# Kernel tuning notes

Measured on AMD Instinct MI355X. Metric: run time of the kernel, lower is better.

Reference implementation:

```python
import jax, jax.numpy as jnp
import numpy as np

N_NODES = 100000
N_EDGES = 800000
DIM = 300
N_GRAPHS = 64
ATOM_VOCAB = 41
WORD_VOCAB = 10000


def setup_inputs() -> dict:
    key = jax.random.key(0)
    ks = jax.random.split(key, 7)
    atoms = jax.random.randint(ks[0], (N_NODES,), 0, ATOM_VOCAB)
    words = jax.random.randint(ks[1], (N_NODES,), 0, WORD_VOCAB)
    x = jnp.stack([atoms, words], axis=-1)  # [N,2] int indices
    edge_index = jax.random.randint(ks[2], (2, N_EDGES), 0, N_NODES)
    batch = jnp.sort(jax.random.randint(ks[3], (N_NODES,), 0, N_GRAPHS))
    atom_table = jax.random.normal(ks[4], (ATOM_VOCAB, DIM), dtype=jnp.float32) * 0.02
    word_table = jax.random.normal(ks[5], (WORD_VOCAB, DIM), dtype=jnp.float32) * 0.02
    W = jax.random.normal(ks[6], (DIM, DIM), dtype=jnp.float32) / np.sqrt(DIM)
    b = jnp.zeros((DIM,), dtype=jnp.float32)
    return {"x": x, "edge_index": edge_index, "batch": batch,
            "atom_table": atom_table, "word_table": word_table,
            "W": W, "b": b, "num_hops": 3}


def reference(x, edge_index, batch, atom_table, word_table, W, b, num_hops):
    n = x.shape[0]
    # GCNConv: add self-loops, symmetric degree normalization
    loops = jnp.arange(n)
    src = jnp.concatenate([edge_index[0], loops])  # [E+N]
    dst = jnp.concatenate([edge_index[1], loops])
    deg = jax.ops.segment_sum(jnp.ones_like(dst, dtype=W.dtype), dst, num_segments=n)
    dinv = jnp.where(deg > 0, jax.lax.rsqrt(deg), 0.0)
    norm = dinv[src] * dinv[dst]  # [E+N]

    # embed_nodes: atom embedding + word embedding
    h = atom_table[x[:, 0]] + word_table[x[:, 1]]  # [N, D]

    # num_hops applications of the SAME GCNConv (shared W, b)
    for _ in range(num_hops):
        hw = h @ W  # [N, D]
        msg = hw[src] * norm[:, None]  # [E+N, D]
        h = jax.ops.segment_sum(msg, dst, num_segments=n) + b

    # global_mean_pool over batch assignment
    sums = jax.ops.segment_sum(h, batch, num_segments=N_GRAPHS)  # [G, D]
    cnt = jax.ops.segment_sum(jnp.ones((n,), h.dtype), batch, num_segments=N_GRAPHS)
    return sums / jnp.maximum(cnt, 1.0)[:, None]
```

## Files before the change

kernel.cpp:

```cpp
#include <hip/hip_runtime.h>
#include <hip/hip_fp16.h>

#define NG 64
#define NGRAPH_C 64

#define RSZ 12500
#define RSZP 6250
#define NC_MS 64
#define MSB 1024

#define VOC 10000
#define KPAD 10240
#define NKC 40
#define WGK 256

__device__ __forceinline__ unsigned f_as_u(float f) { union { float f; unsigned u; } c; c.f = f; return c.u; }
__device__ __forceinline__ float u_as_f(unsigned u) { union { unsigned u; float f; } c; c.u = u; return c.f; }

__device__ __forceinline__ int xcc_id() {
    unsigned x;
    asm volatile("s_getreg_b32 %0, hwreg(HW_REG_XCC_ID)" : "=s"(x));
    return (int)(x & 7u);
}

union H4 { uint2 u2; __half h[4]; };

__global__ __launch_bounds__(MSB) void k_mscount(const int* __restrict__ src, const int* __restrict__ dst,
                                                 unsigned* __restrict__ rep_in,
                                                 unsigned* __restrict__ rep_src,
                                                 int e, int n, int chunk, int npairs) {
    __shared__ unsigned hin[RSZP];
    __shared__ unsigned hsrc[RSZP];
    int c = blockIdx.x % NC_MS;
    int r = blockIdx.x / NC_MS;
    int base = r * RSZ;
    int t = threadIdx.x;
    for (int w = t; w < RSZP; w += MSB) { hin[w] = 0u; hsrc[w] = 0u; }
    __syncthreads();
    int e0 = c * chunk, e1 = min(e, e0 + chunk);
    for (int i = e0 + t; i < e1; i += MSB) {
        int s = src[i], d = dst[i];
        unsigned ud = (unsigned)(d - base);
        unsigned us = (unsigned)(s - base);
        if (ud < (unsigned)RSZ) atomicAdd(&hin[ud >> 1], 1u << ((ud & 1) * 16));
        if (us < (unsigned)RSZ) atomicAdd(&hsrc[us >> 1], 1u << ((us & 1) * 16));
    }
    __syncthreads();
    int lim = min(RSZ, n - base);
    if (lim <= 0) return;
    int plim = (lim + 1) >> 1;
    unsigned* gin  = rep_in  + (size_t)c * npairs + (base >> 1);
    unsigned* gsrc = rep_src + (size_t)c * npairs + (base >> 1);
    for (int w = t; w < plim; w += MSB) { gin[w] = hin[w]; gsrc[w] = hsrc[w]; }
}

__global__ __launch_bounds__(256) void k_msreduce(const unsigned* __restrict__ rep_in,
                                                  unsigned* __restrict__ rep_src,
                                                  float* __restrict__ dinv,
                                                  unsigned* __restrict__ counts_src,
                                                  int n, int npairs) {
    int i2 = blockIdx.x * 256 + threadIdx.x;
    if (i2 >= npairs) return;
    unsigned slo = 0, shi = 0, rlo = 0, rhi = 0;
#pragma unroll 4
    for (int c = 0; c < NC_MS; ++c) {
        unsigned vi = rep_in[(size_t)c * npairs + i2];
        slo += vi & 0xFFFFu; shi += vi >> 16;
        unsigned vs = rep_src[(size_t)c * npairs + i2];
        rep_src[(size_t)c * npairs + i2] = rlo | (rhi << 16);
        rlo += vs & 0xFFFFu; rhi += vs >> 16;
    }
    int i = i2 * 2;
    dinv[i] = rsqrtf((float)(slo + 1u));
    counts_src[i] = rlo;
    if (i + 1 < n) {
        dinv[i + 1] = rsqrtf((float)(shi + 1u));
        counts_src[i + 1] = rhi;
    }
}

__global__ __launch_bounds__(256) void k_blocksum(const unsigned* __restrict__ counts,
                                                  unsigned* __restrict__ partials, int n) {
    __shared__ unsigned s[256];
    int base = blockIdx.x * 1024;
    unsigned sum = 0;
    for (int j = threadIdx.x; j < 1024; j += 256) {
        int i = base + j;
        sum += (i < n) ? counts[i] : 0u;
    }
    s[threadIdx.x] = sum;
    __syncthreads();
    for (int off = 128; off > 0; off >>= 1) {
        if (threadIdx.x < (unsigned)off) s[threadIdx.x] += s[threadIdx.x + off];
        __syncthreads();
    }
    if (threadIdx.x == 0) partials[blockIdx.x] = s[0];
}

__global__ __launch_bounds__(128) void k_scanpartials(unsigned* __restrict__ partials, int nb) {
    __shared__ unsigned s[128];
    int t = threadIdx.x;
    s[t] = (t < nb) ? partials[t] : 0u;
    __syncthreads();
    if (t == 0) {
        unsigned run = 0;
        for (int i = 0; i < nb; ++i) { unsigned v = s[i]; s[i] = run; run += v; }
    }
    __syncthreads();
    if (t < nb) partials[t] = s[t];
}

__global__ __launch_bounds__(256) void k_scanblock(const unsigned* __restrict__ counts,
                                                   const unsigned* __restrict__ partials,
                                                   unsigned* __restrict__ row_start, int n) {
    __shared__ unsigned s[256];
    int base = blockIdx.x * 1024;
    int t = threadIdx.x;
    unsigned v[4];
    unsigned tsum = 0;
#pragma unroll
    for (int j = 0; j < 4; ++j) {
        int i = base + t * 4 + j;
        v[j] = (i < n) ? counts[i] : 0u;
        tsum += v[j];
    }
    s[t] = tsum;
    __syncthreads();
    for (int off = 1; off < 256; off <<= 1) {
        unsigned x = (t >= off) ? s[t - off] : 0u;
        __syncthreads();
        s[t] += x;
        __syncthreads();
    }
    unsigned excl = (t > 0 ? s[t - 1] : 0u) + partials[blockIdx.x];
#pragma unroll
    for (int j = 0; j < 4; ++j) {
        int i = base + t * 4 + j;
        if (i < n) {
            row_start[i] = excl;
            excl += v[j];
            if (i == n - 1) row_start[n] = excl;
        }
    }
}

__global__ __launch_bounds__(MSB) void k_msfill(const int* __restrict__ src, const int* __restrict__ dst,
                                                const int* __restrict__ batch,
                                                const unsigned* __restrict__ row_start,
                                                const unsigned* __restrict__ pref,
                                                const float* __restrict__ dinv,
                                                uint2* __restrict__ euv,
                                                int e, int n, int chunk, int npairs) {
    __shared__ unsigned cur[RSZP];
    int c = blockIdx.x % NC_MS;
    int r = blockIdx.x / NC_MS;
    int base = r * RSZ;
    int t = threadIdx.x;
    for (int w = t; w < RSZP; w += MSB) cur[w] = 0u;
    __syncthreads();
    int e0 = c * chunk, e1 = min(e, e0 + chunk);
    const unsigned* prefc = pref + (size_t)c * npairs;
    for (int i = e0 + t; i < e1; i += MSB) {
        int s = src[i];
        unsigned us = (unsigned)(s - base);
        if (us < (unsigned)RSZ) {
            int d = dst[i];
            unsigned sh = (us & 1) * 16;
            unsigned old = atomicAdd(&cur[us >> 1], 1u << sh);
            unsigned slot = (old >> sh) & 0xFFFFu;
            unsigned p16 = (prefc[(unsigned)s >> 1] >> ((s & 1) * 16)) & 0xFFFFu;
            unsigned pos = row_start[s] + p16 + slot;
            uint2 pv;
            pv.x = (unsigned)d | ((unsigned)batch[d] << 17);
            pv.y = f_as_u(dinv[s] * dinv[d]);
            euv[pos] = pv;
        }
    }
}

__global__ __launch_bounds__(256) void k_wcount(const int* __restrict__ x,
                                                unsigned* __restrict__ wcnt, int n) {
    int j = blockIdx.x * 256 + threadIdx.x;
    if (j >= n) return;
    atomicAdd(&wcnt[x[2 * j + 1]], 1u);
}

__global__ __launch_bounds__(256) void k_wfill(const int* __restrict__ x,
                                               const unsigned* __restrict__ wstart,
                                               unsigned* __restrict__ wcur,
                                               unsigned* __restrict__ sorted, int n) {
    int j = blockIdx.x * 256 + threadIdx.x;
    if (j >= n) return;
    int w = x[2 * j + 1];
    unsigned pos = wstart[w] + atomicAdd(&wcur[w], 1u);
    sorted[pos] = (unsigned)j;
}

__global__ __launch_bounds__(256) void k_twfill(const __half* __restrict__ Y3,
                                                const unsigned* __restrict__ sorted,
                                                const unsigned* __restrict__ wstart,
                                                float* __restrict__ tw) {
    int w = blockIdx.x * 4 + (threadIdx.x >> 6);
    int g = threadIdx.x & 63;
    if (w >= VOC) return;
    unsigned i0 = wstart[w], i1 = wstart[w + 1];
    float s = 0.f;
    unsigned i = i0;
    for (; i + 2 <= i1; i += 2) {
        unsigned j0 = sorted[i], j1 = sorted[i + 1];
        s += __half2float(Y3[(size_t)j0 * NG + g]) + __half2float(Y3[(size_t)j1 * NG + g]);
    }
    if (i < i1) {
        unsigned j0 = sorted[i];
        s += __half2float(Y3[(size_t)j0 * NG + g]);
    }
    tw[(size_t)w * NG + g] = s;
}

__global__ __launch_bounds__(128) void k_gstart(const int* __restrict__ batch,
                                                int* __restrict__ gstart, int n, int ngraph) {
    int g = threadIdx.x;
    if (g > ngraph) return;
    if (g == ngraph) { gstart[g] = n; return; }
    int lo = 0, hi = n;
    while (lo < hi) {
        int mid = (lo + hi) >> 1;
        if (batch[mid] < g) lo = mid + 1; else hi = mid;
    }
    gstart[g] = lo;
}

__global__ __launch_bounds__(256) void k_y1(const int* __restrict__ batch,
                                            const float* __restrict__ dinv,
                                            const unsigned* __restrict__ row_start,
                                            const uint2* __restrict__ euv,
                                            __half* __restrict__ Y1, int n) {
    int idx = blockIdx.x * 256 + threadIdx.x;
    if (idx >= n * 16) return;
    int j = idx >> 4;
    int c4 = idx & 15;
    int cb = c4 * 4;
    float a0 = 0.f, a1 = 0.f, a2 = 0.f, a3 = 0.f;
    {
        int bj = batch[j];
        float dj = dinv[j];
        float sn = dj * dj;
        a0 += (bj == cb + 0) ? sn : 0.f;
        a1 += (bj == cb + 1) ? sn : 0.f;
        a2 += (bj == cb + 2) ? sn : 0.f;
        a3 += (bj == cb + 3) ? sn : 0.f;
    }
    unsigned e0 = row_start[j], e1 = row_start[j + 1];
    unsigned e = e0;
    for (; e + 4 <= e1; e += 4) {
        uint2 p0 = euv[e], p1 = euv[e + 1], p2 = euv[e + 2], p3 = euv[e + 3];
        int b0 = (int)(p0.x >> 17), b1 = (int)(p1.x >> 17);
        int b2 = (int)(p2.x >> 17), b3 = (int)(p3.x >> 17);
        float v0 = u_as_f(p0.y), v1 = u_as_f(p1.y);
        float v2 = u_as_f(p2.y), v3 = u_as_f(p3.y);
        a0 += ((b0 == cb + 0) ? v0 : 0.f) + ((b1 == cb + 0) ? v1 : 0.f)
            + ((b2 == cb + 0) ? v2 : 0.f) + ((b3 == cb + 0) ? v3 : 0.f);
        a1 += ((b0 == cb + 1) ? v0 : 0.f) + ((b1 == cb + 1) ? v1 : 0.f)
            + ((b2 == cb + 1) ? v2 : 0.f) + ((b3 == cb + 1) ? v3 : 0.f);
        a2 += ((b0 == cb + 2) ? v0 : 0.f) + ((b1 == cb + 2) ? v1 : 0.f)
            + ((b2 == cb + 2) ? v2 : 0.f) + ((b3 == cb + 2) ? v3 : 0.f);
        a3 += ((b0 == cb + 3) ? v0 : 0.f) + ((b1 == cb + 3) ? v1 : 0.f)
            + ((b2 == cb + 3) ? v2 : 0.f) + ((b3 == cb + 3) ? v3 : 0.f);
    }
    for (; e < e1; ++e) {
        uint2 p = euv[e];
        int bd = (int)(p.x >> 17);
        float v = u_as_f(p.y);
        a0 += (bd == cb + 0) ? v : 0.f;
        a1 += (bd == cb + 1) ? v : 0.f;
        a2 += (bd == cb + 2) ? v : 0.f;
        a3 += (bd == cb + 3) ? v : 0.f;
    }
    H4 o;
    o.h[0] = __float2half(a0); o.h[1] = __float2half(a1);
    o.h[2] = __float2half(a2); o.h[3] = __float2half(a3);
    *(uint2*)&Y1[(size_t)j * NG + cb] = o.u2;
}

__global__ __launch_bounds__(256) void k_yprop(const __half* __restrict__ Yin,
                                               const float* __restrict__ dinv,
                                               const unsigned* __restrict__ row_start,
                                               const uint2* __restrict__ euv,
                                               __half* __restrict__ Yout, int n) {
    int idx = blockIdx.x * 256 + threadIdx.x;
    if (idx >= n * 16) return;
    int j = idx >> 4;
    int c4 = idx & 15;
    int cb = c4 * 4;
    float dj = dinv[j];
    float sn = dj * dj;
    H4 s; s.u2 = *(const uint2*)&Yin[(size_t)j * NG + cb];
    float a0 = sn * __half2float(s.h[0]);
    float a1 = sn * __half2float(s.h[1]);
    float a2 = sn * __half2float(s.h[2]);
    float a3 = sn * __half2float(s.h[3]);
    unsigned e0 = row_start[j], e1 = row_start[j + 1];
    unsigned e = e0;
    for (; e + 4 <= e1; e += 4) {
        uint2 p0 = euv[e], p1 = euv[e + 1], p2 = euv[e + 2], p3 = euv[e + 3];
        float v0 = u_as_f(p0.y), v1 = u_as_f(p1.y);
        float v2 = u_as_f(p2.y), v3 = u_as_f(p3.y);
        H4 m0; m0.u2 = *(const uint2*)&Yin[(size_t)(p0.x & 0x1FFFFu) * NG + cb];
        H4 m1; m1.u2 = *(const uint2*)&Yin[(size_t)(p1.x & 0x1FFFFu) * NG + cb];
        H4 m2; m2.u2 = *(const uint2*)&Yin[(size_t)(p2.x & 0x1FFFFu) * NG + cb];
        H4 m3; m3.u2 = *(const uint2*)&Yin[(size_t)(p3.x & 0x1FFFFu) * NG + cb];
        a0 += v0 * __half2float(m0.h[0]) + v1 * __half2float(m1.h[0])
            + v2 * __half2float(m2.h[0]) + v3 * __half2float(m3.h[0]);
        a1 += v0 * __half2float(m0.h[1]) + v1 * __half2float(m1.h[1])
            + v2 * __half2float(m2.h[1]) + v3 * __half2float(m3.h[1]);
        a2 += v0 * __half2float(m0.h[2]) + v1 * __half2float(m1.h[2])
            + v2 * __half2float(m2.h[2]) + v3 * __half2float(m3.h[2]);
        a3 += v0 * __half2float(m0.h[3]) + v1 * __half2float(m1.h[3])
            + v2 * __half2float(m2.h[3]) + v3 * __half2float(m3.h[3]);
    }
    for (; e < e1; ++e) {
        uint2 p0 = euv[e];
        float v0 = u_as_f(p0.y);
        H4 m0; m0.u2 = *(const uint2*)&Yin[(size_t)(p0.x & 0x1FFFFu) * NG + cb];
        a0 += v0 * __half2float(m0.h[0]);
        a1 += v0 * __half2float(m0.h[1]);
        a2 += v0 * __half2float(m0.h[2]);
        a3 += v0 * __half2float(m0.h[3]);
    }
    H4 o;
    o.h[0] = __float2half(a0); o.h[1] = __float2half(a1);
    o.h[2] = __float2half(a2); o.h[3] = __float2half(a3);
    *(uint2*)&Yout[(size_t)j * NG + cb] = o.u2;
}

__global__ __launch_bounds__(256) void k_colsumh(const __half* __restrict__ Y,
                                                 float* __restrict__ su8, int n) {
    __shared__ float red[16][NG];
    int t = threadIdx.x;
    int cg = t & 15;
    int sr = t >> 4;
    float a0 = 0.f, a1 = 0.f, a2 = 0.f, a3 = 0.f;
    int stride = gridDim.x * 16;
    for (int j = blockIdx.x * 16 + sr; j < n; j += stride) {
        H4 v; v.u2 = *(const uint2*)&Y[(size_t)j * NG + cg * 4];
        a0 += __half2float(v.h[0]);
        a1 += __half2float(v.h[1]);
        a2 += __half2float(v.h[2]);
        a3 += __half2float(v.h[3]);
    }
    red[sr][cg * 4 + 0] = a0;
    red[sr][cg * 4 + 1] = a1;
    red[sr][cg * 4 + 2] = a2;
    red[sr][cg * 4 + 3] = a3;
    __syncthreads();
    if (t < NG) {
        float s = 0.f;
#pragma unroll
        for (int q = 0; q < 16; ++q) s += red[q][t];
        int r = xcc_id();
        __hip_atomic_fetch_add(&su8[r * NG + t], s,
                               __ATOMIC_RELAXED, __HIP_MEMORY_SCOPE_WORKGROUP);
    }
}

__global__ __launch_bounds__(1024) void k_ta(const __half* __restrict__ Y3,
                                             const int* __restrict__ x,
                                             float* __restrict__ ta, int n) {
    __shared__ float lta[41 * NG];
    int t = threadIdx.x;
    for (int i = t; i < 41 * NG; i += 1024) lta[i] = 0.f;
    __syncthreads();
    int g = t & 63;
    int sv = t >> 6;
    int stride = gridDim.x * 16;
    for (int j = blockIdx.x * 16 + sv; j < n; j += stride) {
        float y = __half2float(Y3[(size_t)j * NG + g]);
        int a = x[2 * j];
        atomicAdd(&lta[a * NG + g], y);
    }
    __syncthreads();
    for (int i = t; i < 41 * NG; i += 1024) atomicAdd(&ta[i], lta[i]);
}

__global__ __launch_bounds__(256) void k_wgemm2(const float* __restrict__ T,
                                                const float* __restrict__ Tab,
                                                float* __restrict__ Gpart) {
    __shared__ float Asm[32 * 64];
    __shared__ float Bsm[32 * 64];
    const int t = threadIdx.x;
    const int tg = t >> 4;
    const int tc = t & 15;
    const int c0 = blockIdx.x * 64;
    const int kb = blockIdx.y * WGK;

    float acc[4][4] = {};

    for (int sub = 0; sub < WGK / 32; ++sub) {
        int kbase = kb + sub * 32;
#pragma unroll
        for (int r2 = 0; r2 < 2; ++r2) {
            int idx4 = r2 * 256 + t;
            int k = idx4 >> 4, g4 = idx4 & 15;
            float4 v = *(const float4*)&T[(size_t)(kbase + k) * 64 + g4 * 4];
            *(float4*)&Asm[k * 64 + g4 * 4] = v;
        }
#pragma unroll
        for (int r2 = 0; r2 < 2; ++r2) {
            int idx4 = r2 * 256 + t;
            int k = idx4 >> 4, c4i = idx4 & 15;
            int gk = kbase + k;
            int cb2 = c0 + c4i * 4;
            float4 v;
            if (gk < VOC && cb2 + 3 < 300) {
                v = *(const float4*)&Tab[(size_t)gk * 300 + cb2];
            } else {
                float tmp[4];
#pragma unroll
                for (int q = 0; q < 4; ++q)
                    tmp[q] = (gk < VOC && cb2 + q < 300) ? Tab[(size_t)gk * 300 + cb2 + q] : 0.f;
                v.x = tmp[0]; v.y = tmp[1]; v.z = tmp[2]; v.w = tmp[3];
            }
            *(float4*)&Bsm[k * 64 + c4i * 4] = v;
        }
        __syncthreads();
#pragma unroll 8
        for (int k = 0; k < 32; ++k) {
            float4 a4 = *(const float4*)&Asm[k * 64 + tg * 4];
            float4 b4 = *(const float4*)&Bsm[k * 64 + tc * 4];
            float a[4] = {a4.x, a4.y, a4.z, a4.w};
            float b[4] = {b4.x, b4.y, b4.z, b4.w};
#pragma unroll
            for (int i = 0; i < 4; ++i)
#pragma unroll
                for (int jj = 0; jj < 4; ++jj) acc[i][jj] += a[i] * b[jj];
        }
        __syncthreads();
    }

    float* gp = Gpart + (size_t)blockIdx.y * (NG * 300);
#pragma unroll
    for (int i = 0; i < 4; ++i) {
        int g = tg * 4 + i;
#pragma unroll
        for (int jj = 0; jj < 4; ++jj) {
            int c = c0 + tc * 4 + jj;
            if (c < 300) gp[g * 300 + c] = acc[i][jj];
        }
    }
}

__global__ __launch_bounds__(256) void k_greduce(const float* __restrict__ Gpart,
                                                 float* __restrict__ G0) {
    int k = blockIdx.x * 256 + threadIdx.x;
    if (k >= NG * 300) return;
    int p0 = blockIdx.y * (NKC / 8);
    int p1 = p0 + (NKC / 8);
    float s = 0.f;
    for (int p = p0; p < p1; ++p) s += Gpart[(size_t)p * (NG * 300) + k];
    atomicAdd(&G0[k], s);
}

__global__ __launch_bounds__(256) void k_agemm(const float* __restrict__ T,
                                               const float* __restrict__ Tab,
                                               float* __restrict__ G0) {
    int j = blockIdx.x * 256 + threadIdx.x;
    if (j >= NG * 300) return;
    int g = j / 300, c = j - g * 300;
    float acc = 0.f;
#pragma unroll
    for (int k = 0; k < 41; ++k) acc += T[(size_t)k * NG + g] * Tab[(size_t)k * 300 + c];
    atomicAdd(&G0[j], acc);
}

__global__ __launch_bounds__(256) void k_smm(const float* __restrict__ A,
                                             const float* __restrict__ W,
                                             float* __restrict__ C) {
    int j = blockIdx.x * 256 + threadIdx.x;
    if (j >= NG * 300) return;
    int g = j / 300, c = j - g * 300;
    int k0 = blockIdx.y * 60;
    float acc = 0.f;
#pragma unroll 1
    for (int k = k0; k < k0 + 60; k += 4) {
        float a0 = A[g * 300 + k + 0], a1 = A[g * 300 + k + 1];
        float a2 = A[g * 300 + k + 2], a3 = A[g * 300 + k + 3];
        float w0 = W[(k + 0) * 300 + c], w1 = W[(k + 1) * 300 + c];
        float w2 = W[(k + 2) * 300 + c], w3 = W[(k + 3) * 300 + c];
        acc += a0 * w0 + a1 * w1 + a2 * w2 + a3 * w3;
    }
    atomicAdd(&C[j], acc);
}

__global__ __launch_bounds__(256) void k_vec(const float* __restrict__ vin,
                                             const float* __restrict__ W,
                                             float* __restrict__ r_out) {
    int c = blockIdx.x * 256 + threadIdx.x;
    if (c >= 300) return;
    int k0 = blockIdx.y * 75;
    float acc = 0.f;
    for (int k = k0; k < k0 + 75; ++k) acc += vin[k] * W[k * 300 + c];
    atomicAdd(&r_out[c], acc);
}

__global__ __launch_bounds__(256) void k_out(const float* __restrict__ T3,
                                             const float* __restrict__ su1,
                                             const float* __restrict__ su2,
                                             const int* __restrict__ gstart,
                                             const float* __restrict__ r1,
                                             const float* __restrict__ r2,
                                             const float* __restrict__ b,
                                             float* __restrict__ out) {
    int j = blockIdx.x * 256 + threadIdx.x;
    if (j >= NG * 300) return;
    int g = j / 300, c = j - g * 300;
    int cnt = gstart[g + 1] - gstart[g];
    float s1 = 0.f, s2 = 0.f;
#pragma unroll
    for (int r = 0; r < 8; ++r) {
        s1 += su1[r * NG + g];
        s2 += su2[r * NG + g];
    }
    float v = T3[j] + s2 * r2[c] + s1 * r1[c] + (float)cnt * b[c];
    out[j] = v / (float)(cnt > 0 ? cnt : 1);
}

extern "C" void kernel_launch(void* const* d_in, const int* in_sizes, int n_in,
                              void* d_out, int out_size, void* d_ws, size_t ws_size,
                              hipStream_t stream) {
    const int*   x     = (const int*)d_in[0];
    const int*   ei    = (const int*)d_in[1];
    const int*   batch = (const int*)d_in[2];
    const float* at    = (const float*)d_in[3];
    const float* wt    = (const float*)d_in[4];
    const float* W     = (const float*)d_in[5];
    const float* b     = (const float*)d_in[6];

    const int n = in_sizes[0] / 2;
    const int e = in_sizes[1] / 2;

    char* ws = (char*)d_ws;
    size_t off = 0;
    auto carve = [&](size_t bytes) {
        void* p = ws + off;
        off += (bytes + 255) & ~(size_t)255;
        return p;
    };
    __half*   Y1        = (__half*)carve((size_t)n * NG * 2);
    __half*   Y2        = (__half*)carve((size_t)n * NG * 2);
    __half*   Y3        = (__half*)carve((size_t)n * NG * 2);
    uint2*    euv       = (uint2*)carve((size_t)e * 8);
    float*    dinv      = (float*)carve((size_t)n * 4);
    unsigned* counts_src= (unsigned*)carve((size_t)n * 4);
    unsigned* row_start = (unsigned*)carve((size_t)(n + 1) * 4);
    unsigned* partials  = (unsigned*)carve(1024 * 4);
    int*      gstart    = (int*)carve(65 * 4);
    unsigned* wstart    = (unsigned*)carve((size_t)(VOC + 1) * 4);
    unsigned* sorted    = (unsigned*)carve((size_t)n * 4);
    char*     zB0       = (char*)carve(0);
    float*    su1       = (float*)carve((size_t)8 * NG * 4);
    float*    su2       = (float*)carve((size_t)8 * NG * 4);
    float*    ta        = (float*)carve((size_t)41 * NG * 4);
    float*    tw        = (float*)carve((size_t)KPAD * NG * 4);
    float*    G0        = (float*)carve((size_t)NG * 300 * 4);
    float*    r1        = (float*)carve(300 * 4);
    float*    r2        = (float*)carve(300 * 4);
    float*    T1        = (float*)carve((size_t)NG * 300 * 4);
    float*    T2        = (float*)carve((size_t)NG * 300 * 4);
    float*    T3        = (float*)carve((size_t)NG * 300 * 4);
    unsigned* wcnt      = (unsigned*)carve((size_t)VOC * 4);
    unsigned* wcur      = (unsigned*)carve((size_t)VOC * 4);
    char*     zB1       = (char*)carve(0);

    const int* src = ei;
    const int* dst = ei + e;

    unsigned* rep_in  = (unsigned*)Y1;
    unsigned* rep_src = (unsigned*)Y2;
    float*    Gpart   = (float*)Y1;

    hipMemsetAsync(zB0, 0, (size_t)(zB1 - zB0), stream);

    const int npairs = (n + 1) / 2;
    const int NRng   = (n + RSZ - 1) / RSZ;
    const int chunk  = (e + NC_MS - 1) / NC_MS;

    k_mscount<<<NRng * NC_MS, MSB, 0, stream>>>(src, dst, rep_in, rep_src, e, n, chunk, npairs);
    k_msreduce<<<(npairs + 255) / 256, 256, 0, stream>>>(rep_in, rep_src, dinv, counts_src, n, npairs);
    int NB = (n + 1023) / 1024;
    k_blocksum<<<NB, 256, 0, stream>>>(counts_src, partials, n);
    k_scanpartials<<<1, 128, 0, stream>>>(partials, NB);
    k_scanblock<<<NB, 256, 0, stream>>>(counts_src, partials, row_start, n);
    k_msfill<<<NRng * NC_MS, MSB, 0, stream>>>(src, dst, batch, row_start, rep_src, dinv, euv, e, n, chunk, npairs);
    k_gstart<<<1, 128, 0, stream>>>(batch, gstart, n, NGRAPH_C);

    int nb256 = (n + 255) / 256;
    k_wcount<<<nb256, 256, 0, stream>>>(x, wcnt, n);
    int NBW = (VOC + 1023) / 1024;
    k_blocksum<<<NBW, 256, 0, stream>>>(wcnt, partials, VOC);
    k_scanpartials<<<1, 128, 0, stream>>>(partials, NBW);
    k_scanblock<<<NBW, 256, 0, stream>>>(wcnt, partials, wstart, VOC);
    k_wfill<<<nb256, 256, 0, stream>>>(x, wstart, wcur, sorted, n);

    int yb = (n * 16 + 255) / 256;
    k_y1<<<yb, 256, 0, stream>>>(batch, dinv, row_start, euv, Y1, n);
    k_colsumh<<<512, 256, 0, stream>>>(Y1, su1, n);
    k_yprop<<<yb, 256, 0, stream>>>(Y1, dinv, row_start, euv, Y2, n);
    k_colsumh<<<512, 256, 0, stream>>>(Y2, su2, n);
    k_yprop<<<yb, 256, 0, stream>>>(Y2, dinv, row_start, euv, Y3, n);

    k_ta<<<512, 1024, 0, stream>>>(Y3, x, ta, n);
    k_twfill<<<(VOC + 3) / 4, 256, 0, stream>>>(Y3, sorted, wstart, tw);
    {
        dim3 gw(5, NKC);
        k_wgemm2<<<gw, 256, 0, stream>>>(tw, wt, Gpart);
        dim3 gr((NG * 300 + 255) / 256, 8);
        k_greduce<<<gr, 256, 0, stream>>>(Gpart, G0);
    }
    k_agemm<<<(NG * 300 + 255) / 256, 256, 0, stream>>>(ta, at, G0);

    {
        dim3 gs((NG * 300 + 255) / 256, 5);
        k_smm<<<gs, 256, 0, stream>>>(G0, W, T1);
        k_smm<<<gs, 256, 0, stream>>>(T1, W, T2);
        k_smm<<<gs, 256, 0, stream>>>(T2, W, T3);
        dim3 gv(2, 4);
        k_vec<<<gv, 256, 0, stream>>>(b, W, r1);
        k_vec<<<gv, 256, 0, stream>>>(r1, W, r2);
    }

    k_out<<<(NG * 300 + 255) / 256, 256, 0, stream>>>(T3, su1, su2, gstart, r1, r2, b, (float*)d_out);
}
```

Baseline: 352.3 us.

## Replace atomic atom-table accumulation with counting-sort segmented reduction; halve wgemm K-chunk

```diff
diff --git a/kernel.cpp b/kernel.cpp
--- a/kernel.cpp
+++ b/kernel.cpp
@@ -11,8 +11,12 @@
 
 #define VOC 10000
 #define KPAD 10240
-#define NKC 40
-#define WGK 256
+#define NKC 80
+#define WGK 128
+
+#define NATOM 41
+#define NC_A 128
+#define ASL 128
 
 __device__ __forceinline__ unsigned f_as_u(float f) { union { float f; unsigned u; } c; c.f = f; return c.u; }
 __device__ __forceinline__ float u_as_f(unsigned u) { union { unsigned u; float f; } c; c.u = u; return c.f; }
@@ -215,6 +219,97 @@
         s += __half2float(Y3[(size_t)j0 * NG + g]);
     }
     tw[(size_t)w * NG + g] = s;
+}
+
+__global__ __launch_bounds__(256) void k_amscount(const int* __restrict__ x,
+                                                  unsigned* __restrict__ rep_a,
+                                                  int n, int chunk) {
+    __shared__ unsigned h[NATOM];
+    int c = blockIdx.x;
+    int t = threadIdx.x;
+    if (t < NATOM) h[t] = 0u;
+    __syncthreads();
+    int j0 = c * chunk, j1 = min(n, j0 + chunk);
+    for (int j = j0 + t; j < j1; j += 256) atomicAdd(&h[x[2 * j]], 1u);
+    __syncthreads();
+    if (t < NATOM) rep_a[c * NATOM + t] = h[t];
+}
+
+__global__ __launch_bounds__(64) void k_amsscan(unsigned* __restrict__ rep_a,
+                                                unsigned* __restrict__ astart, int n) {
+    __shared__ unsigned tot[NATOM];
+    int t = threadIdx.x;
+    if (t < NATOM) {
+        unsigned run = 0;
+        for (int c = 0; c < NC_A; ++c) {
+            unsigned v = rep_a[c * NATOM + t];
+            rep_a[c * NATOM + t] = run;
+            run += v;
+        }
+        tot[t] = run;
+    }
+    __syncthreads();
+    if (t == 0) {
+        unsigned run = 0;
+        for (int a = 0; a < NATOM; ++a) { astart[a] = run; run += tot[a]; }
+        astart[NATOM] = run;
+    }
+}
+
+__global__ __launch_bounds__(256) void k_amsfill(const int* __restrict__ x,
+                                                 const unsigned* __restrict__ astart,
+                                                 const unsigned* __restrict__ rep_a,
+                                                 unsigned* __restrict__ asorted,
+                                                 int n, int chunk) {
+    __shared__ unsigned cur[NATOM];
+    __shared__ unsigned base[NATOM];
+    int c = blockIdx.x;
+    int t = threadIdx.x;
+    if (t < NATOM) {
+        cur[t] = 0u;
+        base[t] = astart[t] + rep_a[c * NATOM + t];
+    }
+    __syncthreads();
+    int j0 = c * chunk, j1 = min(n, j0 + chunk);
+    for (int j = j0 + t; j < j1; j += 256) {
+        int a = x[2 * j];
+        unsigned slot = atomicAdd(&cur[a], 1u);
+        asorted[base[a] + slot] = (unsigned)j;
+    }
+}
+
+__global__ __launch_bounds__(256) void k_tafill(const __half* __restrict__ Y3,
+                                                const unsigned* __restrict__ asorted,
+                                                const unsigned* __restrict__ astart,
+                                                float* __restrict__ tap) {
+    int wid = blockIdx.x * 4 + (threadIdx.x >> 6);
+    if (wid >= NATOM * ASL) return;
+    int a  = wid >> 7;
+    int sl = wid & (ASL - 1);
+    int g  = threadIdx.x & 63;
+    unsigned i0 = astart[a], i1 = astart[a + 1];
+    unsigned len = i1 - i0;
+    unsigned lo = i0 + (unsigned)((unsigned long long)len * sl / ASL);
+    unsigned hi = i0 + (unsigned)((unsigned long long)len * (sl + 1) / ASL);
+    float s = 0.f;
+    unsigned i = lo;
+    for (; i + 2 <= hi; i += 2) {
+        unsigned j0 = asorted[i], j1 = asorted[i + 1];
+        s += __half2float(Y3[(size_t)j0 * NG + g]) + __half2float(Y3[(size_t)j1 * NG + g]);
+    }
+    if (i < hi) s += __half2float(Y3[(size_t)asorted[i] * NG + g]);
+    tap[((size_t)a * ASL + sl) * NG + g] = s;
+}
+
+__global__ __launch_bounds__(256) void k_tareduce(const float* __restrict__ tap,
+                                                  float* __restrict__ ta) {
+    int i = blockIdx.x * 256 + threadIdx.x;
+    if (i >= NATOM * NG) return;
+    int a = i >> 6;
+    int g = i & 63;
+    float s = 0.f;
+    for (int sl = 0; sl < ASL; ++sl) s += tap[((size_t)a * ASL + sl) * NG + g];
+    ta[i] = s;
 }
 
 __global__ __launch_bounds__(128) void k_gstart(const int* __restrict__ batch,
@@ -363,25 +458,6 @@
     }
 }
 
-__global__ __launch_bounds__(1024) void k_ta(const __half* __restrict__ Y3,
-                                             const int* __restrict__ x,
-                                             float* __restrict__ ta, int n) {
-    __shared__ float lta[41 * NG];
-    int t = threadIdx.x;
-    for (int i = t; i < 41 * NG; i += 1024) lta[i] = 0.f;
-    __syncthreads();
-    int g = t & 63;
-    int sv = t >> 6;
-    int stride = gridDim.x * 16;
-    for (int j = blockIdx.x * 16 + sv; j < n; j += stride) {
-        float y = __half2float(Y3[(size_t)j * NG + g]);
-        int a = x[2 * j];
-        atomicAdd(&lta[a * NG + g], y);
-    }
-    __syncthreads();
-    for (int i = t; i < 41 * NG; i += 1024) atomicAdd(&ta[i], lta[i]);
-}
-
 __global__ __launch_bounds__(256) void k_wgemm2(const float* __restrict__ T,
                                                 const float* __restrict__ Tab,
                                                 float* __restrict__ Gpart) {
@@ -556,10 +632,14 @@
     int*      gstart    = (int*)carve(65 * 4);
     unsigned* wstart    = (unsigned*)carve((size_t)(VOC + 1) * 4);
     unsigned* sorted    = (unsigned*)carve((size_t)n * 4);
+    unsigned* asorted   = (unsigned*)carve((size_t)n * 4);
+    unsigned* astart    = (unsigned*)carve((NATOM + 1) * 4);
+    unsigned* rep_a     = (unsigned*)carve((size_t)NC_A * NATOM * 4);
+    float*    tap       = (float*)carve((size_t)NATOM * ASL * NG * 4);
     char*     zB0       = (char*)carve(0);
     float*    su1       = (float*)carve((size_t)8 * NG * 4);
     float*    su2       = (float*)carve((size_t)8 * NG * 4);
-    float*    ta        = (float*)carve((size_t)41 * NG * 4);
+    float*    ta        = (float*)carve((size_t)NATOM * NG * 4);
     float*    tw        = (float*)carve((size_t)KPAD * NG * 4);
     float*    G0        = (float*)carve((size_t)NG * 300 * 4);
     float*    r1        = (float*)carve(300 * 4);
@@ -583,6 +663,7 @@
     const int npairs = (n + 1) / 2;
     const int NRng   = (n + RSZ - 1) / RSZ;
     const int chunk  = (e + NC_MS - 1) / NC_MS;
+    const int achunk = (n + NC_A - 1) / NC_A;
 
     k_mscount<<<NRng * NC_MS, MSB, 0, stream>>>(src, dst, rep_in, rep_src, e, n, chunk, npairs);
     k_msreduce<<<(npairs + 255) / 256, 256, 0, stream>>>(rep_in, rep_src, dinv, counts_src, n, npairs);
@@ -601,6 +682,10 @@
     k_scanblock<<<NBW, 256, 0, stream>>>(wcnt, partials, wstart, VOC);
     k_wfill<<<nb256, 256, 0, stream>>>(x, wstart, wcur, sorted, n);
 
+    k_amscount<<<NC_A, 256, 0, stream>>>(x, rep_a, n, achunk);
+    k_amsscan<<<1, 64, 0, stream>>>(rep_a, astart, n);
+    k_amsfill<<<NC_A, 256, 0, stream>>>(x, astart, rep_a, asorted, n, achunk);
+
     int yb = (n * 16 + 255) / 256;
     k_y1<<<yb, 256, 0, stream>>>(batch, dinv, row_start, euv, Y1, n);
     k_colsumh<<<512, 256, 0, stream>>>(Y1, su1, n);
@@ -608,7 +693,8 @@
     k_colsumh<<<512, 256, 0, stream>>>(Y2, su2, n);
     k_yprop<<<yb, 256, 0, stream>>>(Y2, dinv, row_start, euv, Y3, n);
 
-    k_ta<<<512, 1024, 0, stream>>>(Y3, x, ta, n);
+    k_tafill<<<(NATOM * ASL + 3) / 4, 256, 0, stream>>>(Y3, asorted, astart, tap);
+    k_tareduce<<<(NATOM * NG + 255) / 256, 256, 0, stream>>>(tap, ta);
     k_twfill<<<(VOC + 3) / 4, 256, 0, stream>>>(Y3, sorted, wstart, tw);
     {
         dim3 gw(5, NKC);
```

Result: faster. 325.3 us (-7.7%).
